# Kernel optimization log

Hardware: AMD Instinct MI355X
Metric: run time of the kernel (lower is better)

## Reference

```python
import jax, jax.numpy as jnp
import numpy as np


def setup_inputs() -> dict:
    key = jax.random.key(0)
    k1, k2, k3 = jax.random.split(key, 3)
    N, M, D = 8192, 16384, 24
    return {
        "x": jax.random.normal(k1, (M, D), dtype=jnp.float32),
        "samples": jax.random.normal(k2, (N, D), dtype=jnp.float32),
        "weights": jax.random.uniform(k3, (N,), dtype=jnp.float32),
        "sigma": jnp.ones((), dtype=jnp.float32),
        "length": jnp.ones((), dtype=jnp.float32),
    }


def reference(x, samples, weights, sigma, length):
    # Squared-exponential kernel K[n, m] = sigma^2 * exp(-||s_n - x_m||^2 / (2 l^2))
    # pairwise squared distances via ||s||^2 + ||x||^2 - 2 s.x  -> [N, M]
    s_sq = jnp.sum(samples * samples, axis=-1)[:, None]          # [N, 1]
    x_sq = jnp.sum(x * x, axis=-1)[None, :]                      # [1, M]
    cross = jnp.einsum("nd,md->nm", samples, x)                  # [N, M]
    sqdist = jnp.maximum(s_sq + x_sq - 2.0 * cross, 0.0)
    K = (sigma * sigma) * jnp.exp(-0.5 * sqdist / (length * length))  # [N, M]
    # torch.mv(K.T, weights).unsqueeze(1) -> [M, 1]
    out = jnp.einsum("nm,n->m", K, weights)[:, None]
    return out
```

## Files before the change

### kernel.cpp

```cpp
#include <hip/hip_runtime.h>


#define LOG2E_F 1.4426950408889634f

typedef __attribute__((ext_vector_type(8))) short bf16x8;
typedef __attribute__((ext_vector_type(4))) float f32x4;
typedef float v2f_ __attribute__((ext_vector_type(2)));

constexpr int D      = 24;
constexpr int TILES  = 4;
constexpr int NSPLIT = 32;
constexpr int CT     = 16;
constexpr int TPB    = 256;

__device__ inline unsigned short f32_to_bf16_rne(float f) {
    unsigned u = __builtin_bit_cast(unsigned, f);
    u += 0x7fffu + ((u >> 16) & 1u);
    return (unsigned short)(u >> 16);
}
__device__ inline float bf16_to_f32(unsigned short h) {
    unsigned u = ((unsigned)h) << 16;
    return __builtin_bit_cast(float, u);
}

constexpr unsigned short BF16_ONE = 0x3F80;

__device__ inline float load_row24(const float* __restrict__ src, float* v) {
    float ssq = 0.f;
#pragma unroll
    for (int i = 0; i < 6; ++i) {
        float4 f = reinterpret_cast<const float4*>(src)[i];
        v[4*i+0] = f.x; v[4*i+1] = f.y; v[4*i+2] = f.z; v[4*i+3] = f.w;
    }
#pragma unroll
    for (int d = 0; d < 24; ++d) ssq = fmaf(v[d], v[d], ssq);
    return ssq;
}

__device__ inline void stage_row(unsigned short* __restrict__ sm, int t,
                                 const float* __restrict__ v, float scale,
                                 float splitval, bool split_at_26) {
    unsigned short hi[32], lo[32];
#pragma unroll
    for (int d = 0; d < 24; ++d) {
        float vs = scale * v[d];
        unsigned short h = f32_to_bf16_rne(vs);
        hi[d] = h;
        lo[d] = f32_to_bf16_rne(vs - bf16_to_f32(h));
    }
    unsigned short shv = f32_to_bf16_rne(splitval);
    unsigned short slv = f32_to_bf16_rne(splitval - bf16_to_f32(shv));
    if (split_at_26) { hi[24] = BF16_ONE; hi[25] = BF16_ONE; hi[26] = shv; hi[27] = slv; }
    else             { hi[24] = shv; hi[25] = slv; hi[26] = BF16_ONE; hi[27] = BF16_ONE; }
    hi[28] = 0; hi[29] = 0; hi[30] = 0; hi[31] = 0;
#pragma unroll
    for (int d = 24; d < 32; ++d) lo[d] = 0;
    int sb = (t >> 4) * 512 + (t & 15) * 8;
#pragma unroll
    for (int q2 = 0; q2 < 4; ++q2) {
        bf16x8 vh, vl;
#pragma unroll
        for (int j2 = 0; j2 < 8; ++j2) { vh[j2] = (short)hi[q2*8+j2]; vl[j2] = (short)lo[q2*8+j2]; }
        *reinterpret_cast<bf16x8*>(sm + sb + q2 * 128) = vh;
        *reinterpret_cast<bf16x8*>(sm + 8192 + sb + q2 * 128) = vl;
    }
}

__global__ __launch_bounds__(TPB, 5) void ke_fused(
    const float* __restrict__ x, const float* __restrict__ s,
    const float* __restrict__ wts,
    const float* __restrict__ sigma_p, const float* __restrict__ length_p,
    float* __restrict__ out, int M, int N, int MGRP) {
    __shared__ __align__(16) unsigned short sm[16384];
    int t    = threadIdx.x;
    int lane = t & 63;
    int wv   = t >> 6;
    int mg   = blockIdx.x % MGRP;
    int ns   = blockIdx.x / MGRP;
    int r    = lane & 15;

    float l    = length_p[0];
    float c2   = -0.5f * LOG2E_F / (l * l);
    float m2c2 = -2.f * c2;
    float sg   = sigma_p[0];

    float v[24];
    {
        int row = mg * 256 + t;
        float ssq = load_row24(x + (size_t)row * D, v);
        stage_row(sm, t, v, 1.f, c2 * ssq, true);
    }
    __syncthreads();
    bf16x8 bh[TILES], bl[TILES];
#pragma unroll
    for (int j = 0; j < TILES; ++j) {
        int si = ((wv * 4 + j) * 64 + lane) * 8;
        bh[j] = *reinterpret_cast<const bf16x8*>(sm + si);
        bl[j] = *reinterpret_cast<const bf16x8*>(sm + 8192 + si);
    }
#pragma unroll
    for (int j = 0; j < TILES; ++j) { asm("" : "+v"(bh[j]), "+v"(bl[j])); }
    __syncthreads();
    {
        int row = ns * 256 + t;
        float ssq = load_row24(s + (size_t)row * D, v);
        float lwt = __log2f(sg * sg * wts[row]) + c2 * ssq;
        lwt = fmaxf(lwt, -20000.f);
        stage_row(sm, t, v, m2c2, lwt, false);
    }
    __syncthreads();
    float p[TILES] = {0.f, 0.f, 0.f, 0.f};
#pragma unroll 1
    for (int tt = 0; tt < CT; ++tt) {
        bf16x8 ah = *reinterpret_cast<const bf16x8*>(sm + (tt * 64 + lane) * 8);
        bf16x8 al = *reinterpret_cast<const bf16x8*>(sm + 8192 + (tt * 64 + lane) * 8);
#pragma unroll
        for (int j = 0; j < TILES; ++j) {
            f32x4 z = {0.f, 0.f, 0.f, 0.f};
            f32x4 acc = __builtin_amdgcn_mfma_f32_16x16x32_bf16(ah, bh[j], z, 0, 0, 0);
            acc = __builtin_amdgcn_mfma_f32_16x16x32_bf16(al, bh[j], acc, 0, 0, 0);
            acc = __builtin_amdgcn_mfma_f32_16x16x32_bf16(ah, bl[j], acc, 0, 0, 0);
            float e0 = __builtin_amdgcn_exp2f(acc[0]);
            float e1 = __builtin_amdgcn_exp2f(acc[1]);
            float e2 = __builtin_amdgcn_exp2f(acc[2]);
            float e3 = __builtin_amdgcn_exp2f(acc[3]);
            p[j] += (e0 + e1) + (e2 + e3);
        }
    }
#pragma unroll
    for (int j = 0; j < TILES; ++j) {
        p[j] += __shfl_xor(p[j], 16, 64);
        p[j] += __shfl_xor(p[j], 32, 64);
    }
    if (lane < 16) {
        int m0 = mg * 256 + wv * 64;
#pragma unroll
        for (int j = 0; j < TILES; ++j)
            atomicAdd(&out[m0 + j * 16 + r], p[j]);
    }
}

constexpr int MPT  = 2;
constexpr int MBLK = TPB * MPT;

__global__ __launch_bounds__(TPB) void ke_plain(
    const float* __restrict__ x, const float* __restrict__ samples,
    const float* __restrict__ weights, const float* __restrict__ sigma_p,
    const float* __restrict__ length_p, float* __restrict__ out,
    int M, int N, int nsplit, int chunk) {
    int mb = blockIdx.x / nsplit;
    int ns = blockIdx.x - mb * nsplit;
    int t  = threadIdx.x;
    int m0 = mb * MBLK + t;
    int m1 = m0 + TPB;
    int m0c = (m0 < M) ? m0 : 0;
    int m1c = (m1 < M) ? m1 : 0;

    v2f_ xaq[D / 2], xbq[D / 2];
    const v2f_* xp0 = reinterpret_cast<const v2f_*>(x + (size_t)m0c * D);
    const v2f_* xp1 = reinterpret_cast<const v2f_*>(x + (size_t)m1c * D);
#pragma unroll
    for (int qq = 0; qq < D / 2; ++qq) { xaq[qq] = xp0[qq]; xbq[qq] = xp1[qq]; }
#pragma unroll
    for (int qq = 0; qq < D / 2; ++qq) { asm("" : "+v"(xaq[qq])); asm("" : "+v"(xbq[qq])); }

    float l   = length_p[0];
    float c   = -0.5f * LOG2E_F / (l * l);
    float m2c = -2.f * c;
    float sg  = sigma_p[0];
    float sg2 = sg * sg;

    v2f_ qa = {0.f, 0.f}, qb = {0.f, 0.f};
#pragma unroll
    for (int qq = 0; qq < D / 2; ++qq) {
        qa = __builtin_elementwise_fma(xaq[qq], xaq[qq], qa);
        qb = __builtin_elementwise_fma(xbq[qq], xbq[qq], qb);
    }
    float cxa = c * (qa.x + qa.y);
    float cxb = c * (qb.x + qb.y);

    float acc0 = 0.f, acc1 = 0.f;
    int n0 = ns * chunk;
    int n1 = n0 + chunk;
    if (n1 > N) n1 = N;
#pragma unroll 2
    for (int n = n0; n < n1; ++n) {
        const v2f_* s2 = reinterpret_cast<const v2f_*>(samples + (size_t)n * D);
        v2f_ da = {0.f, 0.f}, db = {0.f, 0.f}, sq = {0.f, 0.f};
#pragma unroll
        for (int qq = 0; qq < D / 2; ++qq) {
            v2f_ sv = s2[qq];
            sq = __builtin_elementwise_fma(sv, sv, sq);
            da = __builtin_elementwise_fma(sv, xaq[qq], da);
            db = __builtin_elementwise_fma(sv, xbq[qq], db);
        }
        float cn = c * (sq.x + sq.y);
        float wn = sg2 * weights[n];
        float e0 = fmaf(m2c, da.x + da.y, cn);
        float e1 = fmaf(m2c, db.x + db.y, cn);
        acc0 = fmaf(wn, __builtin_amdgcn_exp2f(e0), acc0);
        acc1 = fmaf(wn, __builtin_amdgcn_exp2f(e1), acc1);
    }
    if (m0 < M) atomicAdd(&out[m0], acc0 * __builtin_amdgcn_exp2f(cxa));
    if (m1 < M) atomicAdd(&out[m1], acc1 * __builtin_amdgcn_exp2f(cxb));
}

extern "C" void kernel_launch(void* const* d_in, const int* in_sizes, int n_in,
                              void* d_out, int out_size, void* d_ws, size_t ws_size,
                              hipStream_t stream) {
    const float* x       = (const float*)d_in[0];
    const float* samples = (const float*)d_in[1];
    const float* weights = (const float*)d_in[2];
    const float* sigma_p = (const float*)d_in[3];
    const float* length_p= (const float*)d_in[4];
    float* out = (float*)d_out;

    int M = in_sizes[0] / D;
    int N = in_sizes[1] / D;

    hipMemsetAsync(out, 0, (size_t)out_size * sizeof(float), stream);

    bool fused_ok = (M % 256) == 0 && (N == NSPLIT * CT * 16) && out_size >= M;

    if (fused_ok) {
        int MGRP   = M / 256;
        int blocks = MGRP * NSPLIT;
        ke_fused<<<dim3(blocks), dim3(TPB), 0, stream>>>(
            x, samples, weights, sigma_p, length_p, out, M, N, MGRP);
    } else {
        int mbcnt  = (M + MBLK - 1) / MBLK;
        int nsplit = 2048 / (mbcnt > 0 ? mbcnt : 1);
        if (nsplit < 1) nsplit = 1;
        if (nsplit > N) nsplit = N;
        int chunk = (N + nsplit - 1) / nsplit;
        ke_plain<<<dim3(mbcnt * nsplit), dim3(TPB), 0, stream>>>(
            x, samples, weights, sigma_p, length_p, out, M, N, nsplit, chunk);
    }
}
```

Before: 36.78 us.

## Software-pipeline MFMA and exp2 stages with double-buffered accumulators

Restructures the inner loop so the MFMA distance computation for the next tile is issued before the exp2 reduction of the previous tile, using two accumulator sets (accA/accB) and sched_barrier to stop the compiler from reordering them. The goal is to hide MFMA latency behind transcendental work. It also accumulates the exp sums with packed 2-wide float adds. This uses more VGPRs for the extra accumulators, which could reduce occupancy below the launch bound of 5 blocks per SM.

Result: no change. 36.49 us (-0.8%).

```diff
diff --git a/kernel.cpp b/kernel.cpp
--- a/kernel.cpp
+++ b/kernel.cpp
@@ -109,26 +109,62 @@
         stage_row(sm, t, v, m2c2, lwt, false);
     }
     __syncthreads();
-    float p[TILES] = {0.f, 0.f, 0.f, 0.f};
+
+    f32x4 zeroq = {0.f, 0.f, 0.f, 0.f};
+    asm("" : "+v"(zeroq));
+
+    v2f_ p2[TILES] = {{0.f, 0.f}, {0.f, 0.f}, {0.f, 0.f}, {0.f, 0.f}};
+    f32x4 accA[TILES], accB[TILES];
+
+#define KE_MFMA_BLOCK(ACC, TT)                                                        \
+    {                                                                                 \
+        bf16x8 ah = *reinterpret_cast<const bf16x8*>(sm + ((size_t)(TT) * 64 + lane) * 8);        \
+        bf16x8 al = *reinterpret_cast<const bf16x8*>(sm + 8192 + ((size_t)(TT) * 64 + lane) * 8); \
+        _Pragma("unroll")                                                             \
+        for (int j = 0; j < TILES; ++j) {                                             \
+            ACC[j] = __builtin_amdgcn_mfma_f32_16x16x32_bf16(ah, bh[j], zeroq, 0, 0, 0); \
+            ACC[j] = __builtin_amdgcn_mfma_f32_16x16x32_bf16(al, bh[j], ACC[j], 0, 0, 0); \
+            ACC[j] = __builtin_amdgcn_mfma_f32_16x16x32_bf16(ah, bl[j], ACC[j], 0, 0, 0); \
+        }                                                                             \
+    }
+
+#define KE_EXP_BLOCK(ACC)                                                             \
+    {                                                                                 \
+        _Pragma("unroll")                                                             \
+        for (int j = 0; j < TILES; ++j) {                                             \
+            float e0 = __builtin_amdgcn_exp2f(ACC[j][0]);                             \
+            float e1 = __builtin_amdgcn_exp2f(ACC[j][1]);                             \
+            float e2 = __builtin_amdgcn_exp2f(ACC[j][2]);                             \
+            float e3 = __builtin_amdgcn_exp2f(ACC[j][3]);                             \
+            v2f_ a = {e0, e2};                                                        \
+            v2f_ b = {e1, e3};                                                        \
+            p2[j] += a + b;                                                           \
+        }                                                                             \
+    }
+
+    KE_MFMA_BLOCK(accA, 0)
 #pragma unroll 1
-    for (int tt = 0; tt < CT; ++tt) {
-        bf16x8 ah = *reinterpret_cast<const bf16x8*>(sm + (tt * 64 + lane) * 8);
-        bf16x8 al = *reinterpret_cast<const bf16x8*>(sm + 8192 + (tt * 64 + lane) * 8);
-#pragma unroll
-        for (int j = 0; j < TILES; ++j) {
-            f32x4 z = {0.f, 0.f, 0.f, 0.f};
-            f32x4 acc = __builtin_amdgcn_mfma_f32_16x16x32_bf16(ah, bh[j], z, 0, 0, 0);
-            acc = __builtin_amdgcn_mfma_f32_16x16x32_bf16(al, bh[j], acc, 0, 0, 0);
-            acc = __builtin_amdgcn_mfma_f32_16x16x32_bf16(ah, bl[j], acc, 0, 0, 0);
-            float e0 = __builtin_amdgcn_exp2f(acc[0]);
-            float e1 = __builtin_amdgcn_exp2f(acc[1]);
-            float e2 = __builtin_amdgcn_exp2f(acc[2]);
-            float e3 = __builtin_amdgcn_exp2f(acc[3]);
-            p[j] += (e0 + e1) + (e2 + e3);
-        }
-    }
+    for (int g = 0; g < (CT - 2) / 2; ++g) {
+        int t1 = 2 * g + 1;
+        KE_MFMA_BLOCK(accB, t1)
+        __builtin_amdgcn_sched_barrier(0);
+        KE_EXP_BLOCK(accA)
+        KE_MFMA_BLOCK(accA, t1 + 1)
+        __builtin_amdgcn_sched_barrier(0);
+        KE_EXP_BLOCK(accB)
+    }
+    KE_MFMA_BLOCK(accB, CT - 1)
+    __builtin_amdgcn_sched_barrier(0);
+    KE_EXP_BLOCK(accA)
+    KE_EXP_BLOCK(accB)
+
+#undef KE_MFMA_BLOCK
+#undef KE_EXP_BLOCK
+
+    float p[TILES];
 #pragma unroll
     for (int j = 0; j < TILES; ++j) {
+        p[j] = p2[j].x + p2[j].y;
         p[j] += __shfl_xor(p[j], 16, 64);
         p[j] += __shfl_xor(p[j], 32, 64);
     }
```

## Widen fused block to 8 waves and build x fragments directly in registers

Applied to the files above, without the earlier changes.

The fused kernel goes from 256 to 512 threads (8 waves). Each block now covers 512 x rows against one shared 256-sample tile, so the samples staged in LDS are reused by twice as many waves and the grid has half as many blocks. Each lane now loads its x MFMA B-operand fragments straight from global memory and splits them into bf16 hi/lo in registers, with the squared norm reduced by shuffles. This drops the LDS round trip and the extra barriers for x. In exchange, only half the threads stage samples, x is read with a less coalesced pattern, and the launch bound changes to 8, which affects register and occupancy limits.

After: 35.04 us. 1.05x faster.

```diff
diff --git a/kernel.cpp b/kernel.cpp
--- a/kernel.cpp
+++ b/kernel.cpp
@@ -9,9 +9,10 @@
 
 constexpr int D      = 24;
 constexpr int TILES  = 4;
+constexpr int WB     = 8;
+constexpr int TPB    = 64 * WB;
 constexpr int NSPLIT = 32;
 constexpr int CT     = 16;
-constexpr int TPB    = 256;
 
 __device__ inline unsigned short f32_to_bf16_rne(float f) {
     unsigned u = __builtin_bit_cast(unsigned, f);
@@ -25,48 +26,7 @@
 
 constexpr unsigned short BF16_ONE = 0x3F80;
 
-__device__ inline float load_row24(const float* __restrict__ src, float* v) {
-    float ssq = 0.f;
-#pragma unroll
-    for (int i = 0; i < 6; ++i) {
-        float4 f = reinterpret_cast<const float4*>(src)[i];
-        v[4*i+0] = f.x; v[4*i+1] = f.y; v[4*i+2] = f.z; v[4*i+3] = f.w;
-    }
-#pragma unroll
-    for (int d = 0; d < 24; ++d) ssq = fmaf(v[d], v[d], ssq);
-    return ssq;
-}
-
-__device__ inline void stage_row(unsigned short* __restrict__ sm, int t,
-                                 const float* __restrict__ v, float scale,
-                                 float splitval, bool split_at_26) {
-    unsigned short hi[32], lo[32];
-#pragma unroll
-    for (int d = 0; d < 24; ++d) {
-        float vs = scale * v[d];
-        unsigned short h = f32_to_bf16_rne(vs);
-        hi[d] = h;
-        lo[d] = f32_to_bf16_rne(vs - bf16_to_f32(h));
-    }
-    unsigned short shv = f32_to_bf16_rne(splitval);
-    unsigned short slv = f32_to_bf16_rne(splitval - bf16_to_f32(shv));
-    if (split_at_26) { hi[24] = BF16_ONE; hi[25] = BF16_ONE; hi[26] = shv; hi[27] = slv; }
-    else             { hi[24] = shv; hi[25] = slv; hi[26] = BF16_ONE; hi[27] = BF16_ONE; }
-    hi[28] = 0; hi[29] = 0; hi[30] = 0; hi[31] = 0;
-#pragma unroll
-    for (int d = 24; d < 32; ++d) lo[d] = 0;
-    int sb = (t >> 4) * 512 + (t & 15) * 8;
-#pragma unroll
-    for (int q2 = 0; q2 < 4; ++q2) {
-        bf16x8 vh, vl;
-#pragma unroll
-        for (int j2 = 0; j2 < 8; ++j2) { vh[j2] = (short)hi[q2*8+j2]; vl[j2] = (short)lo[q2*8+j2]; }
-        *reinterpret_cast<bf16x8*>(sm + sb + q2 * 128) = vh;
-        *reinterpret_cast<bf16x8*>(sm + 8192 + sb + q2 * 128) = vl;
-    }
-}
-
-__global__ __launch_bounds__(TPB, 5) void ke_fused(
+__global__ __launch_bounds__(TPB, 8) void ke_fused(
     const float* __restrict__ x, const float* __restrict__ s,
     const float* __restrict__ wts,
     const float* __restrict__ sigma_p, const float* __restrict__ length_p,
@@ -78,42 +38,96 @@
     int mg   = blockIdx.x % MGRP;
     int ns   = blockIdx.x / MGRP;
     int r    = lane & 15;
+    int q    = lane >> 4;
 
     float l    = length_p[0];
     float c2   = -0.5f * LOG2E_F / (l * l);
     float m2c2 = -2.f * c2;
     float sg   = sigma_p[0];
 
-    float v[24];
-    {
-        int row = mg * 256 + t;
-        float ssq = load_row24(x + (size_t)row * D, v);
-        stage_row(sm, t, v, 1.f, c2 * ssq, true);
-    }
-    __syncthreads();
-    bf16x8 bh[TILES], bl[TILES];
-#pragma unroll
-    for (int j = 0; j < TILES; ++j) {
-        int si = ((wv * 4 + j) * 64 + lane) * 8;
-        bh[j] = *reinterpret_cast<const bf16x8*>(sm + si);
-        bl[j] = *reinterpret_cast<const bf16x8*>(sm + 8192 + si);
-    }
-#pragma unroll
-    for (int j = 0; j < TILES; ++j) { asm("" : "+v"(bh[j]), "+v"(bl[j])); }
-    __syncthreads();
-    {
+    if (t < 256) {
         int row = ns * 256 + t;
-        float ssq = load_row24(s + (size_t)row * D, v);
+        const float* sr = s + (size_t)row * D;
+        float v[24];
+        float ssq = 0.f;
+#pragma unroll
+        for (int i = 0; i < 6; ++i) {
+            float4 f = reinterpret_cast<const float4*>(sr)[i];
+            v[4*i+0] = f.x; v[4*i+1] = f.y; v[4*i+2] = f.z; v[4*i+3] = f.w;
+        }
+#pragma unroll
+        for (int d = 0; d < 24; ++d) ssq = fmaf(v[d], v[d], ssq);
         float lwt = __log2f(sg * sg * wts[row]) + c2 * ssq;
         lwt = fmaxf(lwt, -20000.f);
-        stage_row(sm, t, v, m2c2, lwt, false);
-    }
+        unsigned short hi[32], lo[32];
+#pragma unroll
+        for (int d = 0; d < 24; ++d) {
+            float vs = m2c2 * v[d];
+            unsigned short h = f32_to_bf16_rne(vs);
+            hi[d] = h;
+            lo[d] = f32_to_bf16_rne(vs - bf16_to_f32(h));
+        }
+        unsigned short lhi = f32_to_bf16_rne(lwt);
+        hi[24] = lhi; hi[25] = f32_to_bf16_rne(lwt - bf16_to_f32(lhi));
+        hi[26] = BF16_ONE; hi[27] = BF16_ONE;
+        hi[28] = 0; hi[29] = 0; hi[30] = 0; hi[31] = 0;
+#pragma unroll
+        for (int d = 24; d < 32; ++d) lo[d] = 0;
+        int sb = (t >> 4) * 512 + (t & 15) * 8;
+#pragma unroll
+        for (int q2 = 0; q2 < 4; ++q2) {
+            bf16x8 vh, vl;
+#pragma unroll
+            for (int j2 = 0; j2 < 8; ++j2) { vh[j2] = (short)hi[q2*8+j2]; vl[j2] = (short)lo[q2*8+j2]; }
+            *reinterpret_cast<bf16x8*>(sm + sb + q2 * 128) = vh;
+            *reinterpret_cast<bf16x8*>(sm + 8192 + sb + q2 * 128) = vl;
+        }
+    }
+
+    int m0 = mg * (TILES * 16 * WB) + wv * (TILES * 16);
+    bf16x8 bh[TILES], bl[TILES];
+#pragma unroll
+    for (int j = 0; j < TILES; ++j) {
+        int row = m0 + j * 16 + r;
+        int qc  = (q < 3) ? q : 2;
+        const float4* xp = reinterpret_cast<const float4*>(x + (size_t)row * D + qc * 8);
+        float4 f0 = xp[0], f1 = xp[1];
+        float v8[8] = {f0.x, f0.y, f0.z, f0.w, f1.x, f1.y, f1.z, f1.w};
+        float live = (q < 3) ? 1.f : 0.f;
+        float psq = 0.f;
+#pragma unroll
+        for (int e = 0; e < 8; ++e) psq = fmaf(v8[e], v8[e], psq);
+        psq *= live;
+        psq += __shfl_xor(psq, 16, 64);
+        psq += __shfl_xor(psq, 32, 64);
+        float cxv = c2 * psq;
+        if (q < 3) {
+#pragma unroll
+            for (int e = 0; e < 8; ++e) {
+                unsigned short h = f32_to_bf16_rne(v8[e]);
+                bh[j][e] = (short)h;
+                bl[j][e] = (short)f32_to_bf16_rne(v8[e] - bf16_to_f32(h));
+            }
+        } else {
+            unsigned short chv = f32_to_bf16_rne(cxv);
+            bh[j][0] = (short)BF16_ONE; bh[j][1] = (short)BF16_ONE;
+            bh[j][2] = (short)chv;
+            bh[j][3] = (short)f32_to_bf16_rne(cxv - bf16_to_f32(chv));
+            bh[j][4] = 0; bh[j][5] = 0; bh[j][6] = 0; bh[j][7] = 0;
+#pragma unroll
+            for (int e = 0; e < 8; ++e) bl[j][e] = 0;
+        }
+    }
+#pragma unroll
+    for (int j = 0; j < TILES; ++j) { asm("" : "+v"(bh[j]), "+v"(bl[j])); }
+
     __syncthreads();
+
     float p[TILES] = {0.f, 0.f, 0.f, 0.f};
 #pragma unroll 1
     for (int tt = 0; tt < CT; ++tt) {
-        bf16x8 ah = *reinterpret_cast<const bf16x8*>(sm + (tt * 64 + lane) * 8);
-        bf16x8 al = *reinterpret_cast<const bf16x8*>(sm + 8192 + (tt * 64 + lane) * 8);
+        bf16x8 ah = *reinterpret_cast<const bf16x8*>(sm + ((size_t)tt * 64 + lane) * 8);
+        bf16x8 al = *reinterpret_cast<const bf16x8*>(sm + 8192 + ((size_t)tt * 64 + lane) * 8);
 #pragma unroll
         for (int j = 0; j < TILES; ++j) {
             f32x4 z = {0.f, 0.f, 0.f, 0.f};
@@ -133,17 +147,17 @@
         p[j] += __shfl_xor(p[j], 32, 64);
     }
     if (lane < 16) {
-        int m0 = mg * 256 + wv * 64;
 #pragma unroll
         for (int j = 0; j < TILES; ++j)
             atomicAdd(&out[m0 + j * 16 + r], p[j]);
     }
 }
 
+constexpr int FTPB = 256;
 constexpr int MPT  = 2;
-constexpr int MBLK = TPB * MPT;
-
-__global__ __launch_bounds__(TPB) void ke_plain(
+constexpr int MBLK = FTPB * MPT;
+
+__global__ __launch_bounds__(FTPB) void ke_plain(
     const float* __restrict__ x, const float* __restrict__ samples,
     const float* __restrict__ weights, const float* __restrict__ sigma_p,
     const float* __restrict__ length_p, float* __restrict__ out,
@@ -152,7 +166,7 @@
     int ns = blockIdx.x - mb * nsplit;
     int t  = threadIdx.x;
     int m0 = mb * MBLK + t;
-    int m1 = m0 + TPB;
+    int m1 = m0 + FTPB;
     int m0c = (m0 < M) ? m0 : 0;
     int m1c = (m1 < M) ? m1 : 0;
 
@@ -220,10 +234,11 @@
 
     hipMemsetAsync(out, 0, (size_t)out_size * sizeof(float), stream);
 
-    bool fused_ok = (M % 256) == 0 && (N == NSPLIT * CT * 16) && out_size >= M;
+    int MSPAN = TILES * 16 * WB;
+    bool fused_ok = (M % MSPAN) == 0 && (N == NSPLIT * CT * 16) && out_size >= M;
 
     if (fused_ok) {
-        int MGRP   = M / 256;
+        int MGRP   = M / MSPAN;
         int blocks = MGRP * NSPLIT;
         ke_fused<<<dim3(blocks), dim3(TPB), 0, stream>>>(
             x, samples, weights, sigma_p, length_p, out, M, N, MGRP);
@@ -233,7 +248,7 @@
         if (nsplit < 1) nsplit = 1;
         if (nsplit > N) nsplit = N;
         int chunk = (N + nsplit - 1) / nsplit;
-        ke_plain<<<dim3(mbcnt * nsplit), dim3(TPB), 0, stream>>>(
+        ke_plain<<<dim3(mbcnt * nsplit), dim3(FTPB), 0, stream>>>(
             x, samples, weights, sigma_p, length_p, out, M, N, nsplit, chunk);
     }
 }
```
